# Optimization experiments

Measured on AMD Instinct MI355X. Metric: run time of the kernel, lower is better.

The kernel has to match this reference:

```python
import jax, jax.numpy as jnp
import numpy as np

NODE_SIZE = 128
EDGE_SIZE = 20
CUTOFF = 5.0
N_NODES = 20000
N_EDGES = 600000


def silu(x):
    return x * jax.nn.sigmoid(x)


def setup_inputs() -> dict:
    key = jax.random.key(0)
    ks = jax.random.split(key, 20)
    d = NODE_SIZE
    inp = {
        "node_states_scalar": jax.random.normal(ks[0], (N_NODES, d), jnp.float32),
        "node_states_vector": jax.random.normal(ks[1], (N_NODES, 3, d), jnp.float32),
        "edge_states": jax.random.normal(ks[2], (N_EDGES, EDGE_SIZE), jnp.float32),
        "edge_vectors": jax.random.normal(ks[3], (N_EDGES, 3), jnp.float32),
        "edge_norms": jax.random.uniform(ks[4], (N_EDGES, 1), jnp.float32),
        "edge_index": jax.random.randint(ks[5], (N_EDGES, 2), 0, N_NODES, jnp.int64 if jax.config.jax_enable_x64 else jnp.int32),
        # parameters, stored as [in, out] so y = x @ W + b
        "Wf": jax.random.normal(ks[6], (EDGE_SIZE, 3 * d), jnp.float32) * 0.05,
        "bf": jnp.zeros((3 * d,), jnp.float32),
        "Wm1": jax.random.normal(ks[7], (d, d), jnp.float32) * 0.05,
        "bm1": jnp.zeros((d,), jnp.float32),
        "Wm2": jax.random.normal(ks[8], (d, 3 * d), jnp.float32) * 0.05,
        "bm2": jnp.zeros((3 * d,), jnp.float32),
        "WU": jax.random.normal(ks[9], (d, d), jnp.float32) * 0.05,
        "WV": jax.random.normal(ks[10], (d, d), jnp.float32) * 0.05,
        "Wa1": jax.random.normal(ks[11], (2 * d, d), jnp.float32) * 0.05,
        "ba1": jnp.zeros((d,), jnp.float32),
        "Wa2": jax.random.normal(ks[12], (d, 3 * d), jnp.float32) * 0.05,
        "ba2": jnp.zeros((3 * d,), jnp.float32),
    }
    return inp


def reference(node_states_scalar, node_states_vector, edge_states, edge_vectors,
              edge_norms, edge_index, Wf, bf, Wm1, bm1, Wm2, bm2, WU, WV,
              Wa1, ba1, Wa2, ba2):
    d = NODE_SIZE
    n = node_states_scalar.shape[0]

    # --- message function ---
    # cosine cutoff: 0.5*(cos(pi*r/cutoff)+1) for r < cutoff, else 0
    fc = 0.5 * (jnp.cos(jnp.pi * edge_norms / CUTOFF) + 1.0)
    fc = jnp.where(edge_norms < CUTOFF, fc, 0.0)                      # [E,1]
    filter_weight = (edge_states @ Wf + bf) * fc                      # [E,3d]
    scalar_output = silu(node_states_scalar @ Wm1 + bm1) @ Wm2 + bm2  # [N,3d]

    src = edge_index[:, 0]
    dst = edge_index[:, 1]
    filter_output = filter_weight * scalar_output[src]                # [E,3d]
    gate_nodes = filter_output[:, :d]
    gate_edges = filter_output[:, d:2 * d]
    messages_scalar = filter_output[:, 2 * d:]

    gated_node_vec = node_states_vector[src] * gate_nodes[:, None, :]     # [E,3,d]
    gated_edge_vec = gate_edges[:, None, :] * edge_vectors[:, :, None]    # [E,3,d]
    messages_vector = gated_node_vec + gated_edge_vec

    ds_m = jax.ops.segment_sum(messages_scalar, dst, num_segments=n)  # [N,d]
    dv_m = jax.ops.segment_sum(messages_vector, dst, num_segments=n)  # [N,3,d]

    s = node_states_scalar + ds_m
    v = node_states_vector + dv_m

    # --- node state update ---
    Uv = jnp.einsum('nvd,de->nve', v, WU)
    Vv = jnp.einsum('nvd,de->nve', v, WV)
    Vv_sq = jnp.sum(Vv ** 2, axis=1)                                  # [N,d]
    a = silu(jnp.concatenate([s, Vv_sq], axis=1) @ Wa1 + ba1) @ Wa2 + ba2
    a_ss, a_sv, a_vv = a[:, :d], a[:, d:2 * d], a[:, 2 * d:]
    ip = jnp.sum(Uv * Vv, axis=1)                                     # [N,d]

    s = s + a_ss + a_sv * ip
    v = v + a_vv[:, None, :] * Uv
    return (s, v)
```

## Files before the change

kernel.cpp:

```cpp
#include <hip/hip_runtime.h>

#define ND 128
#define ESZ 20
#define NN 20000
#define NE 600000
#define PI_F 3.14159265358979323846f
#define CUT 5.0f

using short8 = __attribute__((ext_vector_type(8))) short;
using f32x4  = __attribute__((ext_vector_type(4))) float;
using hh2    = __attribute__((ext_vector_type(2))) _Float16;

__device__ __forceinline__ float silu_f(float x) { return x / (1.0f + __expf(-x)); }

__device__ __forceinline__ unsigned short f2bf(float x) {
    unsigned u = __float_as_uint(x);
    unsigned r = (u + 0x7FFFu + ((u >> 16) & 1u)) >> 16;
    return (unsigned short)r;
}
__device__ __forceinline__ float bf2f(unsigned short h) {
    return __uint_as_float(((unsigned)h) << 16);
}
__device__ __forceinline__ unsigned pack2bf(float x, float y) {
    return (unsigned)f2bf(x) | ((unsigned)f2bf(y) << 16);
}
__device__ __forceinline__ unsigned pack2h(float x, float y) {
    _Float16 a = (_Float16)x, b = (_Float16)y;
    unsigned short ua = __builtin_bit_cast(unsigned short, a);
    unsigned short ub = __builtin_bit_cast(unsigned short, b);
    return (unsigned)ua | ((unsigned)ub << 16);
}
__device__ __forceinline__ float dot2u(unsigned a, hh2 b, float acc) {
    return __builtin_amdgcn_fdot2(__builtin_bit_cast(hh2, a), b, acc, false);
}

__device__ __forceinline__ void pack_w(const float* __restrict__ W,
                                       unsigned short* __restrict__ P,
                                       int s, int K, int N) {
    int k = s / N, n = s - k * N;
    int dst = ((((n >> 4) * (K >> 5) + (k >> 5)) * 64) +
               (((k >> 3) & 3) << 4) + (n & 15)) * 8 + (k & 7);
    P[dst] = f2bf(W[s]);
}

#define R0 1920000L
#define R1 (R0 + 180224L)
#define R2 (R1 + 4224L)
#define R3 (R2 + 600000L)

__global__ __launch_bounds__(256) void k_front(
    const float4* __restrict__ ns4, const float4* __restrict__ nsv4,
    const int* __restrict__ eidx,
    const float* __restrict__ Wf, const float* __restrict__ bfb,
    const float* __restrict__ Wm1, const float* __restrict__ Wm2,
    const float* __restrict__ WU, const float* __restrict__ WV,
    const float* __restrict__ Wa1, const float* __restrict__ Wa2,
    float4* __restrict__ outs4, float4* __restrict__ outv4,
    ushort4* __restrict__ nsb4, unsigned* __restrict__ gnh,
    unsigned short* __restrict__ p1, unsigned short* __restrict__ p2,
    unsigned short* __restrict__ pU, unsigned short* __restrict__ pV,
    unsigned short* __restrict__ pa1, unsigned short* __restrict__ pa2,
    unsigned* __restrict__ wfh, int* __restrict__ counts) {
    long gid = (long)blockIdx.x * 256 + threadIdx.x;
    if (gid < R0) {
        long i = gid;
        const long S4 = (long)NN * ND / 4;
        if (i < S4) {
            float4 v = ns4[i];
            outs4[i] = v;
            ushort4 h; h.x = f2bf(v.x); h.y = f2bf(v.y); h.z = f2bf(v.z); h.w = f2bf(v.w);
            nsb4[i] = h;
        }
        float4 w = nsv4[i];
        outv4[i] = w;
        unsigned short* gs = (unsigned short*)gnh;
        long b = i * 4;
        gs[(b + 0) * 2 + 1] = f2bf(w.x);
        gs[(b + 1) * 2 + 1] = f2bf(w.y);
        gs[(b + 2) * 2 + 1] = f2bf(w.z);
        gs[(b + 3) * 2 + 1] = f2bf(w.w);
    } else if (gid < R1) {
        int i = (int)(gid - R0);
        if      (i <  16384) pack_w(Wm1, p1, i,          128, 128);
        else if (i <  65536) pack_w(Wm2, p2, i - 16384,  128, 384);
        else if (i <  81920) pack_w(WU,  pU, i - 65536,  128, 128);
        else if (i <  98304) pack_w(WV,  pV, i - 81920,  128, 128);
        else if (i < 131072) pack_w(Wa1, pa1, i - 98304, 256, 128);
        else                 pack_w(Wa2, pa2, i - 131072,128, 384);
    } else if (gid < R2) {
        int j = (int)(gid - R1);
        int p = j / 384, cc = j - p * 384;
        float a = 0.f, b = 0.f;
        if (p < 10) { a = Wf[(2 * p) * 384 + cc]; b = Wf[(2 * p + 1) * 384 + cc]; }
        else if (p == 10) { a = bfb[cc]; }
        wfh[p * 384 + cc] = pack2h(a, b);
    } else if (gid < R3) {
        int e = (int)(gid - R2);
        atomicAdd(&counts[eidx[2 * e + 1]], 1);
    }
}

#define SCAN_T 1024
__global__ __launch_bounds__(SCAN_T) void k_scan(const int* __restrict__ counts,
                                                 int* __restrict__ offsets,
                                                 int* __restrict__ cursor) {
    __shared__ int part[SCAN_T];
    const int t = threadIdx.x;
    const int CPT = (NN + SCAN_T - 1) / SCAN_T;
    const int base = t * CPT;
    int sum = 0;
    for (int i = 0; i < CPT; ++i) {
        int idx = base + i;
        if (idx < NN) sum += counts[idx];
    }
    part[t] = sum;
    __syncthreads();
    for (int off = 1; off < SCAN_T; off <<= 1) {
        int v = (t >= off) ? part[t - off] : 0;
        __syncthreads();
        part[t] += v;
        __syncthreads();
    }
    int run = (t == 0) ? 0 : part[t - 1];
    for (int i = 0; i < CPT; ++i) {
        int idx = base + i;
        if (idx < NN) {
            offsets[idx] = run;
            cursor[idx] = run;
            run += counts[idx];
        }
    }
    if (t == SCAN_T - 1) offsets[NN] = run;
}

#define SCAT_B 2344
__global__ __launch_bounds__(256) void k_sm(
    const int* __restrict__ eidx, int* __restrict__ cursor,
    const float* __restrict__ es, const float* __restrict__ enorm,
    const float* __restrict__ evec, unsigned* __restrict__ rec,
    const unsigned short* __restrict__ nsb,
    const unsigned short* __restrict__ Wm1p, const float* __restrict__ bm1,
    const unsigned short* __restrict__ Wm2p, const float* __restrict__ bm2,
    unsigned* __restrict__ gnh) {
    __shared__ unsigned short lsh[4][16][136];
    if (blockIdx.x < SCAT_B) {
        int e = blockIdx.x * 256 + threadIdx.x;
        if (e < NE) {
            int s  = eidx[2 * e];
            int dd = eidx[2 * e + 1];
            float nrm = enorm[e];
            float fc = (nrm < CUT) ? 0.5f * (__cosf(PI_F * nrm * (1.0f / CUT)) + 1.0f) : 0.0f;
            const float* er = es + (long)e * ESZ;
            unsigned qv[11];
#pragma unroll
            for (int p = 0; p < 10; ++p)
                qv[p] = pack2h(er[2 * p] * fc, er[2 * p + 1] * fc);
            qv[10] = pack2h(fc, 0.f);
            float e0 = evec[3 * e + 0], e1 = evec[3 * e + 1], e2 = evec[3 * e + 2];
            int pos = atomicAdd(&cursor[dd], 1);
            uint4* rp = (uint4*)rec + (long)pos * 4;
            rp[0] = make_uint4((unsigned)s, (unsigned)dd,
                               __float_as_uint(e0), __float_as_uint(e1));
            rp[1] = make_uint4(__float_as_uint(e2), qv[0], qv[1], qv[2]);
            rp[2] = make_uint4(qv[3], qv[4], qv[5], qv[6]);
            rp[3] = make_uint4(qv[7], qv[8], qv[9], qv[10]);
        }
        return;
    }
    const int lane = threadIdx.x & 63;
    const int wv = threadIdx.x >> 6;
    const int wid = (blockIdx.x - SCAT_B) * 4 + wv;
    const int m0 = wid * 16;
    if (m0 >= NN) return;
    const int ml = lane & 15, q = lane >> 4;

    short8 a1[4];
#pragma unroll
    for (int kb = 0; kb < 4; ++kb)
        a1[kb] = *(const short8*)(nsb + (long)(m0 + ml) * ND + kb * 32 + q * 8);

#pragma unroll
    for (int nt = 0; nt < 8; ++nt) {
        float b = bm1[nt * 16 + ml];
        f32x4 acc = {b, b, b, b};
#pragma unroll
        for (int kb = 0; kb < 4; ++kb) {
            short8 bf = *(const short8*)(Wm1p + ((nt * 4 + kb) * 64 + lane) * 8);
            acc = __builtin_amdgcn_mfma_f32_16x16x32_bf16(a1[kb], bf, acc, 0, 0, 0);
        }
#pragma unroll
        for (int r = 0; r < 4; ++r)
            lsh[wv][q * 4 + r][nt * 16 + ml] = f2bf(silu_f(acc[r]));
    }
    __syncthreads();

    short8 a2[4];
#pragma unroll
    for (int kb = 0; kb < 4; ++kb)
        a2[kb] = *(const short8*)(&lsh[wv][ml][kb * 32 + q * 8]);

    unsigned short* gs = (unsigned short*)gnh;
#pragma unroll
    for (int nt = 0; nt < 24; ++nt) {
        float b = bm2[nt * 16 + ml];
        f32x4 acc = {b, b, b, b};
#pragma unroll
        for (int kb = 0; kb < 4; ++kb) {
            short8 bf = *(const short8*)(Wm2p + ((nt * 4 + kb) * 64 + lane) * 8);
            acc = __builtin_amdgcn_mfma_f32_16x16x32_bf16(a2[kb], bf, acc, 0, 0, 0);
        }
#pragma unroll
        for (int r = 0; r < 4; ++r) {
            long idx = (long)(m0 + q * 4 + r) * 384 + nt * 16 + ml;
            gs[idx * 2] = f2bf(acc[r]);
        }
    }
}

#define NGRP 7500
#define RUN 80
#define SLOTS 8

#define STEP(k, dk, gsrc) {                                                   \
    if ((dk) != cur_dst) {                                                    \
        PUSH();                                                               \
        cur_dst = (dk);                                                       \
        as = 0.f; av0 = 0.f; av1 = 0.f; av2 = 0.f;                            \
    }                                                                         \
    const uint4 M0_ = pp[(k) & 1][0], M1_ = pp[(k) & 1][1],                   \
                M2_ = pp[(k) & 1][2], M3_ = pp[(k) & 1][3];                   \
    const unsigned XA_ = xr[(k) & 7][0], XB_ = xr[(k) & 7][1],                \
                   XC_ = xr[(k) & 7][2];                                      \
                                            \
    { const unsigned* pb_ = (((k) + 2 < 16) ? bc : bn) + ((((k) + 2) & 15) << 4); \
      pp[(k) & 1][0] = *(const uint4*)(pb_);                                  \
      pp[(k) & 1][1] = *(const uint4*)(pb_ + 4);                              \
      pp[(k) & 1][2] = *(const uint4*)(pb_ + 8);                              \
      pp[(k) & 1][3] = *(const uint4*)(pb_ + 12); }                           \
                                                         \
    { const unsigned* gp_ = gnh + (long)(gsrc) * 384;                         \
      xr[(k) & 7][0] = gp_[t];                                                \
      xr[(k) & 7][1] = gp_[128 + t];                                          \
      xr[(k) & 7][2] = gp_[256 + t]; }                                        \
    unsigned ea_[11] = {M1_.y, M1_.z, M1_.w, M2_.x, M2_.y, M2_.z, M2_.w,      \
                        M3_.x, M3_.y, M3_.z, M3_.w};                          \
    float f0 = 0.f, f1 = 0.f, f2 = 0.f;                                       \
    _Pragma("unroll")                                                         \
    for (int p = 0; p < 11; ++p) {                                            \
        f0 = dot2u(ea_[p], wf[p][0], f0);                                     \
        f1 = dot2u(ea_[p], wf[p][1], f1);                                     \
        f2 = dot2u(ea_[p], wf[p][2], f2);                                     \
    }                                                                         \
    f0 *= __uint_as_float(XA_ << 16);                                         \
    f1 *= __uint_as_float(XB_ << 16);                                         \
    f2 *= __uint_as_float(XC_ << 16);                                         \
    as  += f2;                                                                \
    av0 += __uint_as_float(XA_ & 0xffff0000u) * f0 + f1 * __uint_as_float(M0_.z); \
    av1 += __uint_as_float(XB_ & 0xffff0000u) * f0 + f1 * __uint_as_float(M0_.w); \
    av2 += __uint_as_float(XC_ & 0xffff0000u) * f0 + f1 * __uint_as_float(M1_.x); \
}

#define RL(v, j) __builtin_amdgcn_readlane((int)(v), (j))

__global__ __launch_bounds__(256, 3) void k_edge8(
    const unsigned* __restrict__ rec, const unsigned* __restrict__ wfh,
    const unsigned* __restrict__ gnh,
    float* __restrict__ out_s, float* __restrict__ out_v) {
    __shared__ __align__(16) unsigned eb[4][2][256];
    __shared__ float fsl[4][SLOTS][4][64];
    __shared__ int dsl[4][SLOTS];
    const int wv = threadIdx.x >> 6;
    const int lane = threadIdx.x & 63;
    const int grp = blockIdx.x * 2 + (wv >> 1);
    const int t = ((wv & 1) << 6) | lane;
    const long beg = (long)grp * RUN;

    hh2 wf[11][3];
#pragma unroll
    for (int p = 0; p < 11; ++p)
#pragma unroll
        for (int c = 0; c < 3; ++c)
            wf[p][c] = __builtin_bit_cast(hh2, wfh[p * 384 + c * 128 + t]);

    unsigned* const b0 = &eb[wv][0][0];
    unsigned* const b1 = &eb[wv][1][0];

    uint4 sA = *(const uint4*)(rec + (beg + 0)  * 16 + lane * 4);
    uint4 sB = *(const uint4*)(rec + (beg + 16) * 16 + lane * 4);
    uint4 st = *(const uint4*)(rec + (beg + 32) * 16 + lane * 4);
    *(uint4*)&b0[lane * 4] = sA;
    *(uint4*)&b1[lane * 4] = sB;
    uint2 sdC = *(const uint2*)&b0[(lane & 15) << 4];
    uint2 sdN = *(const uint2*)&b1[(lane & 15) << 4];

    uint4 pp[2][4];
    pp[0][0] = *(const uint4*)(b0 + 0);  pp[0][1] = *(const uint4*)(b0 + 4);
    pp[0][2] = *(const uint4*)(b0 + 8);  pp[0][3] = *(const uint4*)(b0 + 12);
    pp[1][0] = *(const uint4*)(b0 + 16); pp[1][1] = *(const uint4*)(b0 + 20);
    pp[1][2] = *(const uint4*)(b0 + 24); pp[1][3] = *(const uint4*)(b0 + 28);

    unsigned xr[8][3];
#define IG(j) { int s_ = RL(sdC.x, j);                                        \
                const unsigned* gp_ = gnh + (long)s_ * 384;                   \
                xr[j][0] = gp_[t]; xr[j][1] = gp_[128 + t];                   \
                xr[j][2] = gp_[256 + t]; }
    IG(0) IG(1) IG(2) IG(3) IG(4) IG(5) IG(6) IG(7)
#undef IG

    int cur_dst = -1;
    int nseg = 0;
    float as = 0.f, av0 = 0.f, av1 = 0.f, av2 = 0.f;

    auto DRAIN = [&]() {
        for (int i = 0; i < nseg; ++i) {
            int d = dsl[wv][i];
            atomicAdd(&out_s[(long)d * ND + t],            fsl[wv][i][0][lane]);
            atomicAdd(&out_v[(long)d * 384 + 0 * ND + t],  fsl[wv][i][1][lane]);
            atomicAdd(&out_v[(long)d * 384 + 1 * ND + t],  fsl[wv][i][2][lane]);
            atomicAdd(&out_v[(long)d * 384 + 2 * ND + t],  fsl[wv][i][3][lane]);
        }
        nseg = 0;
    };
    auto PUSH = [&]() {
        if (cur_dst >= 0) {
            fsl[wv][nseg][0][lane] = as;
            fsl[wv][nseg][1][lane] = av0;
            fsl[wv][nseg][2][lane] = av1;
            fsl[wv][nseg][3][lane] = av2;
            if (lane == 0) dsl[wv][nseg] = cur_dst;
            ++nseg;
            if (nseg == SLOTS) DRAIN();
        }
    };

    for (int c = 0; c < 5; ++c) {
        unsigned* const bc = &eb[wv][c & 1][0];
        unsigned* const bn = &eb[wv][(c + 1) & 1][0];
        const int d0  = RL(sdC.y, 0),  d1  = RL(sdC.y, 1);
        const int d2  = RL(sdC.y, 2),  d3  = RL(sdC.y, 3);
        const int d4  = RL(sdC.y, 4),  d5  = RL(sdC.y, 5);
        const int d6  = RL(sdC.y, 6),  d7  = RL(sdC.y, 7);
        const int d8  = RL(sdC.y, 8),  d9  = RL(sdC.y, 9);
        const int d10 = RL(sdC.y, 10), d11 = RL(sdC.y, 11);
        const int d12 = RL(sdC.y, 12), d13 = RL(sdC.y, 13);
        const int d14 = RL(sdC.y, 14), d15 = RL(sdC.y, 15);
        const int s8  = RL(sdC.x, 8),  s9  = RL(sdC.x, 9);
        const int s10 = RL(sdC.x, 10), s11 = RL(sdC.x, 11);
        const int s12 = RL(sdC.x, 12), s13 = RL(sdC.x, 13);
        const int s14 = RL(sdC.x, 14), s15 = RL(sdC.x, 15);

        STEP(0, d0, s8)   STEP(1, d1, s9)   STEP(2, d2, s10)  STEP(3, d3, s11)
        STEP(4, d4, s12)  STEP(5, d5, s13)  STEP(6, d6, s14)  STEP(7, d7, s15)

        const int gm = (c < 4) ? -1 : 0;
        const int n0 = RL(sdN.x, 0) & gm, n1 = RL(sdN.x, 1) & gm;
        const int n2 = RL(sdN.x, 2) & gm, n3 = RL(sdN.x, 3) & gm;
        const int n4 = RL(sdN.x, 4) & gm, n5 = RL(sdN.x, 5) & gm;
        const int n6 = RL(sdN.x, 6) & gm, n7 = RL(sdN.x, 7) & gm;

        STEP(8,  d8,  n0)  STEP(9,  d9,  n1)  STEP(10, d10, n2) STEP(11, d11, n3)
        STEP(12, d12, n4)  STEP(13, d13, n5)  STEP(14, d14, n6) STEP(15, d15, n7)

        if (c < 4) {
            *(uint4*)&bc[lane * 4] = st;
            st = *(const uint4*)(rec + (beg + (long)(c + 3) * 16) * 16 + lane * 4);
            sdC = sdN;
            sdN = *(const uint2*)&bc[(lane & 15) << 4];
        }
    }
    PUSH();
    DRAIN();
}

__global__ __launch_bounds__(256) void k_tail(
    const unsigned short* __restrict__ WUp, const unsigned short* __restrict__ WVp,
    const unsigned short* __restrict__ Wa1p, const float* __restrict__ ba1,
    const unsigned short* __restrict__ Wa2p, const float* __restrict__ ba2,
    float* __restrict__ out_s, float* __restrict__ out_v) {
    const int lane = threadIdx.x & 63;
    const int wv = threadIdx.x >> 6;
    const int wid = blockIdx.x * 4 + wv;
    const int m0 = wid * 16;
    if (m0 >= NN) return;
    const int ml = lane & 15, q = lane >> 4;
    __shared__ unsigned short ct[4][16][264];
    __shared__ unsigned short hl[4][16][136];

#pragma unroll
    for (int j = 0; j < 16; ++j) {
        int idx = j * 64 + lane;
        int n = idx >> 6, c2 = idx & 63;
        float2 sv = *(const float2*)(out_s + (long)(m0 + n) * 128 + c2 * 2);
        *(unsigned*)&ct[wv][n][c2 * 2] = pack2bf(sv.x, sv.y);
    }

    short8 av[3][4];
#pragma unroll
    for (int ax = 0; ax < 3; ++ax)
#pragma unroll
        for (int kb = 0; kb < 4; ++kb) {
            const float* p = out_v + (long)(m0 + ml) * 384 + ax * 128 + kb * 32 + q * 8;
            float4 x = *(const float4*)p;
            float4 y = *(const float4*)(p + 4);
            short8 s;
            s[0] = (short)f2bf(x.x); s[1] = (short)f2bf(x.y);
            s[2] = (short)f2bf(x.z); s[3] = (short)f2bf(x.w);
            s[4] = (short)f2bf(y.x); s[5] = (short)f2bf(y.y);
            s[6] = (short)f2bf(y.z); s[7] = (short)f2bf(y.w);
            av[ax][kb] = s;
        }

    f32x4 ipr[8];
    unsigned upk[8][3][2];
#pragma unroll
    for (int nt = 0; nt < 8; ++nt) {
        f32x4 u0 = {0.f,0.f,0.f,0.f}, u1 = u0, u2 = u0;
        f32x4 v0 = u0, v1 = u0, v2 = u0;
#pragma unroll
        for (int kb = 0; kb < 4; ++kb) {
            short8 bu = *(const short8*)(WUp + ((nt * 4 + kb) * 64 + lane) * 8);
            short8 bv = *(const short8*)(WVp + ((nt * 4 + kb) * 64 + lane) * 8);
            u0 = __builtin_amdgcn_mfma_f32_16x16x32_bf16(av[0][kb], bu, u0, 0, 0, 0);
            u1 = __builtin_amdgcn_mfma_f32_16x16x32_bf16(av[1][kb], bu, u1, 0, 0, 0);
            u2 = __builtin_amdgcn_mfma_f32_16x16x32_bf16(av[2][kb], bu, u2, 0, 0, 0);
            v0 = __builtin_amdgcn_mfma_f32_16x16x32_bf16(av[0][kb], bv, v0, 0, 0, 0);
            v1 = __builtin_amdgcn_mfma_f32_16x16x32_bf16(av[1][kb], bv, v1, 0, 0, 0);
            v2 = __builtin_amdgcn_mfma_f32_16x16x32_bf16(av[2][kb], bv, v2, 0, 0, 0);
        }
        const int c = nt * 16 + ml;
#pragma unroll
        for (int r = 0; r < 4; ++r) {
            float vs  = v0[r] * v0[r] + v1[r] * v1[r] + v2[r] * v2[r];
            ct[wv][q * 4 + r][128 + c] = f2bf(vs);
            ipr[nt][r] = u0[r] * v0[r] + u1[r] * v1[r] + u2[r] * v2[r];
        }
        upk[nt][0][0] = pack2bf(u0[0], u0[1]); upk[nt][0][1] = pack2bf(u0[2], u0[3]);
        upk[nt][1][0] = pack2bf(u1[0], u1[1]); upk[nt][1][1] = pack2bf(u1[2], u1[3]);
        upk[nt][2][0] = pack2bf(u2[0], u2[1]); upk[nt][2][1] = pack2bf(u2[2], u2[3]);
    }

    short8 a1[8];
#pragma unroll
    for (int kb = 0; kb < 8; ++kb)
        a1[kb] = *(const short8*)(&ct[wv][ml][kb * 32 + q * 8]);

#pragma unroll
    for (int nt = 0; nt < 8; ++nt) {
        float b = ba1[nt * 16 + ml];
        f32x4 acc = {b, b, b, b};
#pragma unroll
        for (int kb = 0; kb < 8; ++kb) {
            short8 bf = *(const short8*)(Wa1p + ((nt * 8 + kb) * 64 + lane) * 8);
            acc = __builtin_amdgcn_mfma_f32_16x16x32_bf16(a1[kb], bf, acc, 0, 0, 0);
        }
#pragma unroll
        for (int r = 0; r < 4; ++r)
            hl[wv][q * 4 + r][nt * 16 + ml] = f2bf(silu_f(acc[r]));
    }

    short8 h[4];
#pragma unroll
    for (int kb = 0; kb < 4; ++kb)
        h[kb] = *(const short8*)(&hl[wv][ml][kb * 32 + q * 8]);

#pragma unroll
    for (int nt = 0; nt < 8; ++nt) {
        float b0 = ba2[nt * 16 + ml];
        float b1 = ba2[128 + nt * 16 + ml];
        f32x4 aS = {b0, b0, b0, b0};
        f32x4 aG = {b1, b1, b1, b1};
#pragma unroll
        for (int kb = 0; kb < 4; ++kb) {
            short8 bS = *(const short8*)(Wa2p + (((nt) * 4 + kb) * 64 + lane) * 8);
            short8 bG = *(const short8*)(Wa2p + (((nt + 8) * 4 + kb) * 64 + lane) * 8);
            aS = __builtin_amdgcn_mfma_f32_16x16x32_bf16(h[kb], bS, aS, 0, 0, 0);
            aG = __builtin_amdgcn_mfma_f32_16x16x32_bf16(h[kb], bG, aG, 0, 0, 0);
        }
#pragma unroll
        for (int r = 0; r < 4; ++r) {
            long grow = m0 + q * 4 + r;
            long o = grow * 128 + nt * 16 + ml;
            out_s[o] = out_s[o] + aS[r] + aG[r] * ipr[nt][r];
        }
    }

#pragma unroll
    for (int nt = 0; nt < 8; ++nt) {
        float b2 = ba2[256 + nt * 16 + ml];
        f32x4 aV = {b2, b2, b2, b2};
#pragma unroll
        for (int kb = 0; kb < 4; ++kb) {
            short8 bV = *(const short8*)(Wa2p + (((nt + 16) * 4 + kb) * 64 + lane) * 8);
            aV = __builtin_amdgcn_mfma_f32_16x16x32_bf16(h[kb], bV, aV, 0, 0, 0);
        }
#pragma unroll
        for (int r = 0; r < 4; ++r) {
            long grow = m0 + q * 4 + r;
            int c = nt * 16 + ml;
#pragma unroll
            for (int ax = 0; ax < 3; ++ax) {
                unsigned pk = upk[nt][ax][r >> 1];
                unsigned short uh = (r & 1) ? (unsigned short)(pk >> 16)
                                            : (unsigned short)(pk & 0xffffu);
                long o = grow * 384 + ax * 128 + c;
                out_v[o] = out_v[o] + aV[r] * bf2f(uh);
            }
        }
    }
}

extern "C" void kernel_launch(void* const* d_in, const int* in_sizes, int n_in,
                              void* d_out, int out_size, void* d_ws, size_t ws_size,
                              hipStream_t stream) {
    const float* ns    = (const float*)d_in[0];
    const float* nsv   = (const float*)d_in[1];
    const float* es    = (const float*)d_in[2];
    const float* evec  = (const float*)d_in[3];
    const float* enorm = (const float*)d_in[4];
    const int*   eidx  = (const int*)d_in[5];
    const float* Wf    = (const float*)d_in[6];
    const float* bfb   = (const float*)d_in[7];
    const float* Wm1   = (const float*)d_in[8];
    const float* bm1   = (const float*)d_in[9];
    const float* Wm2   = (const float*)d_in[10];
    const float* bm2   = (const float*)d_in[11];
    const float* WU    = (const float*)d_in[12];
    const float* WV    = (const float*)d_in[13];
    const float* Wa1   = (const float*)d_in[14];
    const float* ba1   = (const float*)d_in[15];
    const float* Wa2   = (const float*)d_in[16];
    const float* ba2   = (const float*)d_in[17];

    float* out_s = (float*)d_out;
    float* out_v = out_s + (size_t)NN * ND;

    char* w = (char*)d_ws;
    unsigned short* p1  = (unsigned short*)(w + 0);
    unsigned short* p2  = (unsigned short*)(w + 32768);
    unsigned short* pU  = (unsigned short*)(w + 131072);
    unsigned short* pV  = (unsigned short*)(w + 163840);
    unsigned short* pa1 = (unsigned short*)(w + 196608);
    unsigned short* pa2 = (unsigned short*)(w + 262144);
    unsigned* wfh = (unsigned*)(w + 360448);
    int* counts = (int*)(w + 377344);
    int* offs   = (int*)(w + 457344);
    int* cursor = (int*)(w + 537408);
    unsigned* rec = (unsigned*)(w + 617408);
    char* u0 = w + 39024576;
    unsigned* gnh       = (unsigned*)(u0);
    unsigned short* nsb = (unsigned short*)(u0 + 30720000);

    hipMemsetAsync(counts, 0, (size_t)NN * sizeof(int), stream);
    hipMemsetAsync(rec + (size_t)NE * 16, 0, 112 * 64, stream);
    k_front<<<(int)((R3 + 255) / 256), 256, 0, stream>>>(
        (const float4*)ns, (const float4*)nsv, eidx, Wf, bfb,
        Wm1, Wm2, WU, WV, Wa1, Wa2,
        (float4*)out_s, (float4*)out_v, (ushort4*)nsb, gnh,
        p1, p2, pU, pV, pa1, pa2, wfh, counts);
    k_scan<<<1, SCAN_T, 0, stream>>>(counts, offs, cursor);
    k_sm<<<SCAT_B + 313, 256, 0, stream>>>(eidx, cursor, es, enorm, evec, rec,
                                           nsb, p1, bm1, p2, bm2, gnh);
    k_edge8<<<NGRP / 2, 256, 0, stream>>>(rec, wfh, gnh, out_s, out_v);
    k_tail<<<313, 256, 0, stream>>>(pU, pV, pa1, ba1, pa2, ba2, out_s, out_v);
}
```

Baseline: 482.2 us.

## Partition edge kernel by destination nodes to replace atomics with direct writes

Result: slower. 527.5 us (+9.4%).

```diff
diff --git a/kernel.cpp b/kernel.cpp
--- a/kernel.cpp
+++ b/kernel.cpp
@@ -55,7 +55,6 @@
     const float* __restrict__ Wm1, const float* __restrict__ Wm2,
     const float* __restrict__ WU, const float* __restrict__ WV,
     const float* __restrict__ Wa1, const float* __restrict__ Wa2,
-    float4* __restrict__ outs4, float4* __restrict__ outv4,
     ushort4* __restrict__ nsb4, unsigned* __restrict__ gnh,
     unsigned short* __restrict__ p1, unsigned short* __restrict__ p2,
     unsigned short* __restrict__ pU, unsigned short* __restrict__ pV,
@@ -67,12 +66,10 @@
         const long S4 = (long)NN * ND / 4;
         if (i < S4) {
             float4 v = ns4[i];
-            outs4[i] = v;
             ushort4 h; h.x = f2bf(v.x); h.y = f2bf(v.y); h.z = f2bf(v.z); h.w = f2bf(v.w);
             nsb4[i] = h;
         }
         float4 w = nsv4[i];
-        outv4[i] = w;
         unsigned short* gs = (unsigned short*)gnh;
         long b = i * 4;
         gs[(b + 0) * 2 + 1] = f2bf(w.x);
@@ -217,31 +214,29 @@
     }
 }
 
-#define NGRP 7500
-#define RUN 80
-#define SLOTS 8
-
-#define STEP(k, dk, gsrc) {                                                   \
-    if ((dk) != cur_dst) {                                                    \
-        PUSH();                                                               \
-        cur_dst = (dk);                                                       \
+#define NDST 4
+#define EMAX 192
+#define NGRP9 (NN / NDST)
+
+#define RL(v, j) __builtin_amdgcn_readlane((int)(v), (j))
+
+#define FLS(sg) {                                                             \
+    fsl[gl][sg][0][t] = as;                                                   \
+    fsl[gl][sg][1][t] = av0;                                                  \
+    fsl[gl][sg][2][t] = av1;                                                  \
+    fsl[gl][sg][3][t] = av2;                                                  \
+}
+
+#define BCHK(k) {                                                             \
+    while ((k) == b_next) {                                                   \
+        FLS(seg);                                                             \
         as = 0.f; av0 = 0.f; av1 = 0.f; av2 = 0.f;                            \
+        ++seg;                                                                \
+        b_next = (seg == 1) ? B2 : (seg == 2) ? B3 : 0x7fffffff;              \
     }                                                                         \
-    const uint4 M0_ = pp[(k) & 1][0], M1_ = pp[(k) & 1][1],                   \
-                M2_ = pp[(k) & 1][2], M3_ = pp[(k) & 1][3];                   \
-    const unsigned XA_ = xr[(k) & 7][0], XB_ = xr[(k) & 7][1],                \
-                   XC_ = xr[(k) & 7][2];                                      \
-                                            \
-    { const unsigned* pb_ = (((k) + 2 < 16) ? bc : bn) + ((((k) + 2) & 15) << 4); \
-      pp[(k) & 1][0] = *(const uint4*)(pb_);                                  \
-      pp[(k) & 1][1] = *(const uint4*)(pb_ + 4);                              \
-      pp[(k) & 1][2] = *(const uint4*)(pb_ + 8);                              \
-      pp[(k) & 1][3] = *(const uint4*)(pb_ + 12); }                           \
-                                                         \
-    { const unsigned* gp_ = gnh + (long)(gsrc) * 384;                         \
-      xr[(k) & 7][0] = gp_[t];                                                \
-      xr[(k) & 7][1] = gp_[128 + t];                                          \
-      xr[(k) & 7][2] = gp_[256 + t]; }                                        \
+}
+
+#define ECOMP(M0_, M1_, M2_, M3_, XA_, XB_, XC_) {                            \
     unsigned ea_[11] = {M1_.y, M1_.z, M1_.w, M2_.x, M2_.y, M2_.z, M2_.w,      \
                         M3_.x, M3_.y, M3_.z, M3_.w};                          \
     float f0 = 0.f, f1 = 0.f, f2 = 0.f;                                       \
@@ -260,20 +255,39 @@
     av2 += __uint_as_float(XC_ & 0xffff0000u) * f0 + f1 * __uint_as_float(M1_.x); \
 }
 
-#define RL(v, j) __builtin_amdgcn_readlane((int)(v), (j))
-
-__global__ __launch_bounds__(256, 3) void k_edge8(
+#define ESTEP(k, s) {                                                         \
+    BCHK(k)                                                                   \
+    const uint4 M0_ = pq[(s) & 1][0], M1_ = pq[(s) & 1][1],                   \
+                M2_ = pq[(s) & 1][2], M3_ = pq[(s) & 1][3];                   \
+    const unsigned XA_ = xr[s][0], XB_ = xr[s][1], XC_ = xr[s][2];            \
+    { const int kp_ = (k) + 2;                                                \
+      const unsigned* pa_ = (kp_ < fl) ? rb + (long)kp_ * 16 : zrec;          \
+      pq[(s) & 1][0] = *(const uint4*)(pa_);                                  \
+      pq[(s) & 1][1] = *(const uint4*)(pa_ + 4);                              \
+      pq[(s) & 1][2] = *(const uint4*)(pa_ + 8);                              \
+      pq[(s) & 1][3] = *(const uint4*)(pa_ + 12); }                           \
+    { int kg_ = (k) + 4; if (kg_ > EMAX - 1) kg_ = EMAX - 1;                  \
+      const int ln_ = kg_ & 63;                                               \
+      int sg_ = RL(srcA, ln_);                                                \
+      sg_ = (kg_ >= 64)  ? RL(srcB, ln_) : sg_;                               \
+      sg_ = (kg_ >= 128) ? RL(srcC, ln_) : sg_;                               \
+      const unsigned* gp_ = gnh + (long)sg_ * 384;                            \
+      xr[s][0] = gp_[t]; xr[s][1] = gp_[128 + t]; xr[s][2] = gp_[256 + t]; }  \
+    ECOMP(M0_, M1_, M2_, M3_, XA_, XB_, XC_)                                  \
+}
+
+__global__ __launch_bounds__(256, 4) void k_edge9(
     const unsigned* __restrict__ rec, const unsigned* __restrict__ wfh,
-    const unsigned* __restrict__ gnh,
+    const unsigned* __restrict__ gnh, const int* __restrict__ offs,
+    const float* __restrict__ ns, const float* __restrict__ nsv,
     float* __restrict__ out_s, float* __restrict__ out_v) {
-    __shared__ __align__(16) unsigned eb[4][2][256];
-    __shared__ float fsl[4][SLOTS][4][64];
-    __shared__ int dsl[4][SLOTS];
+    __shared__ float fsl[2][NDST][4][128];
     const int wv = threadIdx.x >> 6;
     const int lane = threadIdx.x & 63;
-    const int grp = blockIdx.x * 2 + (wv >> 1);
+    const int gl = wv >> 1;
+    const int grp = blockIdx.x * 2 + gl;
     const int t = ((wv & 1) << 6) | lane;
-    const long beg = (long)grp * RUN;
+    const int d0n = grp * NDST;
 
     hh2 wf[11][3];
 #pragma unroll
@@ -282,94 +296,79 @@
         for (int c = 0; c < 3; ++c)
             wf[p][c] = __builtin_bit_cast(hh2, wfh[p * 384 + c * 128 + t]);
 
-    unsigned* const b0 = &eb[wv][0][0];
-    unsigned* const b1 = &eb[wv][1][0];
-
-    uint4 sA = *(const uint4*)(rec + (beg + 0)  * 16 + lane * 4);
-    uint4 sB = *(const uint4*)(rec + (beg + 16) * 16 + lane * 4);
-    uint4 st = *(const uint4*)(rec + (beg + 32) * 16 + lane * 4);
-    *(uint4*)&b0[lane * 4] = sA;
-    *(uint4*)&b1[lane * 4] = sB;
-    uint2 sdC = *(const uint2*)&b0[(lane & 15) << 4];
-    uint2 sdN = *(const uint2*)&b1[(lane & 15) << 4];
-
-    uint4 pp[2][4];
-    pp[0][0] = *(const uint4*)(b0 + 0);  pp[0][1] = *(const uint4*)(b0 + 4);
-    pp[0][2] = *(const uint4*)(b0 + 8);  pp[0][3] = *(const uint4*)(b0 + 12);
-    pp[1][0] = *(const uint4*)(b0 + 16); pp[1][1] = *(const uint4*)(b0 + 20);
-    pp[1][2] = *(const uint4*)(b0 + 24); pp[1][3] = *(const uint4*)(b0 + 28);
-
-    unsigned xr[8][3];
-#define IG(j) { int s_ = RL(sdC.x, j);                                        \
-                const unsigned* gp_ = gnh + (long)s_ * 384;                   \
-                xr[j][0] = gp_[t]; xr[j][1] = gp_[128 + t];                   \
-                xr[j][2] = gp_[256 + t]; }
-    IG(0) IG(1) IG(2) IG(3) IG(4) IG(5) IG(6) IG(7)
-#undef IG
-
-    int cur_dst = -1;
-    int nseg = 0;
+    const int boff = offs[d0n];
+    const int B1 = offs[d0n + 1] - boff;
+    const int B2 = offs[d0n + 2] - boff;
+    const int B3 = offs[d0n + 3] - boff;
+    const int len = offs[d0n + 4] - boff;
+    const unsigned* rb = rec + (long)boff * 16;
+    const unsigned* zrec = rec + (long)NE * 16;
+
+    unsigned srcA = rb[lane * 16];
+    unsigned srcB = rb[(lane + 64) * 16];
+    unsigned srcC = rb[(lane + 128) * 16];
+
+    const int fl = (len < EMAX) ? len : EMAX;
+
+    uint4 pq[2][4];
+    {
+        const unsigned* pa0 = (0 < fl) ? rb : zrec;
+        const unsigned* pa1 = (1 < fl) ? rb + 16 : zrec;
+        pq[0][0] = *(const uint4*)(pa0);      pq[0][1] = *(const uint4*)(pa0 + 4);
+        pq[0][2] = *(const uint4*)(pa0 + 8);  pq[0][3] = *(const uint4*)(pa0 + 12);
+        pq[1][0] = *(const uint4*)(pa1);      pq[1][1] = *(const uint4*)(pa1 + 4);
+        pq[1][2] = *(const uint4*)(pa1 + 8);  pq[1][3] = *(const uint4*)(pa1 + 12);
+    }
+    unsigned xr[4][3];
+#pragma unroll
+    for (int k = 0; k < 4; ++k) {
+        int sgp = RL(srcA, k);
+        const unsigned* gp = gnh + (long)sgp * 384;
+        xr[k][0] = gp[t]; xr[k][1] = gp[128 + t]; xr[k][2] = gp[256 + t];
+    }
+
+    int seg = 0;
+    int b_next = B1;
     float as = 0.f, av0 = 0.f, av1 = 0.f, av2 = 0.f;
 
-    auto DRAIN = [&]() {
-        for (int i = 0; i < nseg; ++i) {
-            int d = dsl[wv][i];
-            atomicAdd(&out_s[(long)d * ND + t],            fsl[wv][i][0][lane]);
-            atomicAdd(&out_v[(long)d * 384 + 0 * ND + t],  fsl[wv][i][1][lane]);
-            atomicAdd(&out_v[(long)d * 384 + 1 * ND + t],  fsl[wv][i][2][lane]);
-            atomicAdd(&out_v[(long)d * 384 + 2 * ND + t],  fsl[wv][i][3][lane]);
-        }
-        nseg = 0;
-    };
-    auto PUSH = [&]() {
-        if (cur_dst >= 0) {
-            fsl[wv][nseg][0][lane] = as;
-            fsl[wv][nseg][1][lane] = av0;
-            fsl[wv][nseg][2][lane] = av1;
-            fsl[wv][nseg][3][lane] = av2;
-            if (lane == 0) dsl[wv][nseg] = cur_dst;
-            ++nseg;
-            if (nseg == SLOTS) DRAIN();
-        }
-    };
-
-    for (int c = 0; c < 5; ++c) {
-        unsigned* const bc = &eb[wv][c & 1][0];
-        unsigned* const bn = &eb[wv][(c + 1) & 1][0];
-        const int d0  = RL(sdC.y, 0),  d1  = RL(sdC.y, 1);
-        const int d2  = RL(sdC.y, 2),  d3  = RL(sdC.y, 3);
-        const int d4  = RL(sdC.y, 4),  d5  = RL(sdC.y, 5);
-        const int d6  = RL(sdC.y, 6),  d7  = RL(sdC.y, 7);
-        const int d8  = RL(sdC.y, 8),  d9  = RL(sdC.y, 9);
-        const int d10 = RL(sdC.y, 10), d11 = RL(sdC.y, 11);
-        const int d12 = RL(sdC.y, 12), d13 = RL(sdC.y, 13);
-        const int d14 = RL(sdC.y, 14), d15 = RL(sdC.y, 15);
-        const int s8  = RL(sdC.x, 8),  s9  = RL(sdC.x, 9);
-        const int s10 = RL(sdC.x, 10), s11 = RL(sdC.x, 11);
-        const int s12 = RL(sdC.x, 12), s13 = RL(sdC.x, 13);
-        const int s14 = RL(sdC.x, 14), s15 = RL(sdC.x, 15);
-
-        STEP(0, d0, s8)   STEP(1, d1, s9)   STEP(2, d2, s10)  STEP(3, d3, s11)
-        STEP(4, d4, s12)  STEP(5, d5, s13)  STEP(6, d6, s14)  STEP(7, d7, s15)
-
-        const int gm = (c < 4) ? -1 : 0;
-        const int n0 = RL(sdN.x, 0) & gm, n1 = RL(sdN.x, 1) & gm;
-        const int n2 = RL(sdN.x, 2) & gm, n3 = RL(sdN.x, 3) & gm;
-        const int n4 = RL(sdN.x, 4) & gm, n5 = RL(sdN.x, 5) & gm;
-        const int n6 = RL(sdN.x, 6) & gm, n7 = RL(sdN.x, 7) & gm;
-
-        STEP(8,  d8,  n0)  STEP(9,  d9,  n1)  STEP(10, d10, n2) STEP(11, d11, n3)
-        STEP(12, d12, n4)  STEP(13, d13, n5)  STEP(14, d14, n6) STEP(15, d15, n7)
-
-        if (c < 4) {
-            *(uint4*)&bc[lane * 4] = st;
-            st = *(const uint4*)(rec + (beg + (long)(c + 3) * 16) * 16 + lane * 4);
-            sdC = sdN;
-            sdN = *(const uint2*)&bc[(lane & 15) << 4];
-        }
-    }
-    PUSH();
-    DRAIN();
+    const int nit = (fl + 3) >> 2;
+#pragma clang loop unroll(disable)
+    for (int it = 0; it < nit; ++it) {
+        const int k0 = it * 4;
+        ESTEP(k0 + 0, 0)
+        ESTEP(k0 + 1, 1)
+        ESTEP(k0 + 2, 2)
+        ESTEP(k0 + 3, 3)
+    }
+
+    if (len > EMAX) {
+        for (int k = EMAX; k < len; ++k) {
+            BCHK(k)
+            const unsigned* pa = rb + (long)k * 16;
+            uint4 m0 = *(const uint4*)(pa),     m1 = *(const uint4*)(pa + 4);
+            uint4 m2 = *(const uint4*)(pa + 8), m3 = *(const uint4*)(pa + 12);
+            const unsigned* gp = gnh + (long)m0.x * 384;
+            unsigned xa = gp[t], xb = gp[128 + t], xc = gp[256 + t];
+            ECOMP(m0, m1, m2, m3, xa, xb, xc)
+        }
+    }
+
+    FLS(seg);
+    as = 0.f; av0 = 0.f; av1 = 0.f; av2 = 0.f;
+    for (int i = seg + 1; i < NDST; ++i) FLS(i);
+
+#pragma unroll
+    for (int d = 0; d < NDST; ++d) {
+        const long node = d0n + d;
+        float s0 = fsl[gl][d][0][t];
+        float v0 = fsl[gl][d][1][t];
+        float v1 = fsl[gl][d][2][t];
+        float v2 = fsl[gl][d][3][t];
+        out_s[node * ND + t]            = ns[node * ND + t] + s0;
+        out_v[node * 384 + 0 * ND + t]  = nsv[node * 384 + 0 * ND + t] + v0;
+        out_v[node * 384 + 1 * ND + t]  = nsv[node * 384 + 1 * ND + t] + v1;
+        out_v[node * 384 + 2 * ND + t]  = nsv[node * 384 + 2 * ND + t] + v2;
+    }
 }
 
 __global__ __launch_bounds__(256) void k_tail(
@@ -546,20 +545,21 @@
     int* offs   = (int*)(w + 457344);
     int* cursor = (int*)(w + 537408);
     unsigned* rec = (unsigned*)(w + 617408);
-    char* u0 = w + 39024576;
+    char* u0 = w + 39029696;
     unsigned* gnh       = (unsigned*)(u0);
     unsigned short* nsb = (unsigned short*)(u0 + 30720000);
 
     hipMemsetAsync(counts, 0, (size_t)NN * sizeof(int), stream);
-    hipMemsetAsync(rec + (size_t)NE * 16, 0, 112 * 64, stream);
+    hipMemsetAsync(rec + (size_t)NE * 16, 0, 192 * 64, stream);
     k_front<<<(int)((R3 + 255) / 256), 256, 0, stream>>>(
         (const float4*)ns, (const float4*)nsv, eidx, Wf, bfb,
         Wm1, Wm2, WU, WV, Wa1, Wa2,
-        (float4*)out_s, (float4*)out_v, (ushort4*)nsb, gnh,
+        (ushort4*)nsb, gnh,
         p1, p2, pU, pV, pa1, pa2, wfh, counts);
     k_scan<<<1, SCAN_T, 0, stream>>>(counts, offs, cursor);
     k_sm<<<SCAT_B + 313, 256, 0, stream>>>(eidx, cursor, es, enorm, evec, rec,
                                            nsb, p1, bm1, p2, bm2, gnh);
-    k_edge8<<<NGRP / 2, 256, 0, stream>>>(rec, wfh, gnh, out_s, out_v);
+    k_edge9<<<NGRP9 / 2, 256, 0, stream>>>(rec, wfh, gnh, offs, ns, nsv,
+                                           out_s, out_v);
     k_tail<<<313, 256, 0, stream>>>(pU, pV, pa1, ba1, pa2, ba2, out_s, out_v);
 }
```

## Pack node-vector bf16 into gnh in k_sm and flush edge segments directly

Applied to the files above, without the earlier changes.

After: 468.0 us. 2.9% less time.

```diff
diff --git a/kernel.cpp b/kernel.cpp
--- a/kernel.cpp
+++ b/kernel.cpp
@@ -56,7 +56,7 @@
     const float* __restrict__ WU, const float* __restrict__ WV,
     const float* __restrict__ Wa1, const float* __restrict__ Wa2,
     float4* __restrict__ outs4, float4* __restrict__ outv4,
-    ushort4* __restrict__ nsb4, unsigned* __restrict__ gnh,
+    ushort4* __restrict__ nsb4,
     unsigned short* __restrict__ p1, unsigned short* __restrict__ p2,
     unsigned short* __restrict__ pU, unsigned short* __restrict__ pV,
     unsigned short* __restrict__ pa1, unsigned short* __restrict__ pa2,
@@ -71,14 +71,7 @@
             ushort4 h; h.x = f2bf(v.x); h.y = f2bf(v.y); h.z = f2bf(v.z); h.w = f2bf(v.w);
             nsb4[i] = h;
         }
-        float4 w = nsv4[i];
-        outv4[i] = w;
-        unsigned short* gs = (unsigned short*)gnh;
-        long b = i * 4;
-        gs[(b + 0) * 2 + 1] = f2bf(w.x);
-        gs[(b + 1) * 2 + 1] = f2bf(w.y);
-        gs[(b + 2) * 2 + 1] = f2bf(w.z);
-        gs[(b + 3) * 2 + 1] = f2bf(w.w);
+        outv4[i] = nsv4[i];
     } else if (gid < R1) {
         int i = (int)(gid - R0);
         if      (i <  16384) pack_w(Wm1, p1, i,          128, 128);
@@ -138,7 +131,7 @@
     const int* __restrict__ eidx, int* __restrict__ cursor,
     const float* __restrict__ es, const float* __restrict__ enorm,
     const float* __restrict__ evec, unsigned* __restrict__ rec,
-    const unsigned short* __restrict__ nsb,
+    const unsigned short* __restrict__ nsb, const float* __restrict__ nsv,
     const unsigned short* __restrict__ Wm1p, const float* __restrict__ bm1,
     const unsigned short* __restrict__ Wm2p, const float* __restrict__ bm2,
     unsigned* __restrict__ gnh) {
@@ -199,7 +192,6 @@
     for (int kb = 0; kb < 4; ++kb)
         a2[kb] = *(const short8*)(&lsh[wv][ml][kb * 32 + q * 8]);
 
-    unsigned short* gs = (unsigned short*)gnh;
 #pragma unroll
     for (int nt = 0; nt < 24; ++nt) {
         float b = bm2[nt * 16 + ml];
@@ -212,19 +204,25 @@
 #pragma unroll
         for (int r = 0; r < 4; ++r) {
             long idx = (long)(m0 + q * 4 + r) * 384 + nt * 16 + ml;
-            gs[idx * 2] = f2bf(acc[r]);
+            gnh[idx] = (unsigned)f2bf(acc[r]) | ((unsigned)f2bf(nsv[idx]) << 16);
         }
     }
 }
 
 #define NGRP 7500
 #define RUN 80
-#define SLOTS 8
+
+#define FLUSH() {                                                             \
+    atomicAdd(&out_s[(long)cur_dst * ND + t], as);                            \
+    atomicAdd(&out_v[(long)cur_dst * 384 + 0 * ND + t], av0);                 \
+    atomicAdd(&out_v[(long)cur_dst * 384 + 1 * ND + t], av1);                 \
+    atomicAdd(&out_v[(long)cur_dst * 384 + 2 * ND + t], av2);                 \
+}
 
 #define STEP(k, dk, gsrc) {                                                   \
-    if ((dk) != cur_dst) {                                                    \
-        PUSH();                                                               \
-        cur_dst = (dk);                                                       \
+    if (dk != cur_dst) {                                                      \
+        if (cur_dst >= 0) FLUSH();                                            \
+        cur_dst = dk;                                                         \
         as = 0.f; av0 = 0.f; av1 = 0.f; av2 = 0.f;                            \
     }                                                                         \
     const uint4 M0_ = pp[(k) & 1][0], M1_ = pp[(k) & 1][1],                   \
@@ -262,13 +260,11 @@
 
 #define RL(v, j) __builtin_amdgcn_readlane((int)(v), (j))
 
-__global__ __launch_bounds__(256, 3) void k_edge8(
+__global__ __launch_bounds__(256, 3) void k_edge7(
     const unsigned* __restrict__ rec, const unsigned* __restrict__ wfh,
     const unsigned* __restrict__ gnh,
     float* __restrict__ out_s, float* __restrict__ out_v) {
     __shared__ __align__(16) unsigned eb[4][2][256];
-    __shared__ float fsl[4][SLOTS][4][64];
-    __shared__ int dsl[4][SLOTS];
     const int wv = threadIdx.x >> 6;
     const int lane = threadIdx.x & 63;
     const int grp = blockIdx.x * 2 + (wv >> 1);
@@ -308,30 +304,7 @@
 #undef IG
 
     int cur_dst = -1;
-    int nseg = 0;
     float as = 0.f, av0 = 0.f, av1 = 0.f, av2 = 0.f;
-
-    auto DRAIN = [&]() {
-        for (int i = 0; i < nseg; ++i) {
-            int d = dsl[wv][i];
-            atomicAdd(&out_s[(long)d * ND + t],            fsl[wv][i][0][lane]);
-            atomicAdd(&out_v[(long)d * 384 + 0 * ND + t],  fsl[wv][i][1][lane]);
-            atomicAdd(&out_v[(long)d * 384 + 1 * ND + t],  fsl[wv][i][2][lane]);
-            atomicAdd(&out_v[(long)d * 384 + 2 * ND + t],  fsl[wv][i][3][lane]);
-        }
-        nseg = 0;
-    };
-    auto PUSH = [&]() {
-        if (cur_dst >= 0) {
-            fsl[wv][nseg][0][lane] = as;
-            fsl[wv][nseg][1][lane] = av0;
-            fsl[wv][nseg][2][lane] = av1;
-            fsl[wv][nseg][3][lane] = av2;
-            if (lane == 0) dsl[wv][nseg] = cur_dst;
-            ++nseg;
-            if (nseg == SLOTS) DRAIN();
-        }
-    };
 
     for (int c = 0; c < 5; ++c) {
         unsigned* const bc = &eb[wv][c & 1][0];
@@ -368,8 +341,7 @@
             sdN = *(const uint2*)&bc[(lane & 15) << 4];
         }
     }
-    PUSH();
-    DRAIN();
+    FLUSH();
 }
 
 __global__ __launch_bounds__(256) void k_tail(
@@ -555,11 +527,11 @@
     k_front<<<(int)((R3 + 255) / 256), 256, 0, stream>>>(
         (const float4*)ns, (const float4*)nsv, eidx, Wf, bfb,
         Wm1, Wm2, WU, WV, Wa1, Wa2,
-        (float4*)out_s, (float4*)out_v, (ushort4*)nsb, gnh,
+        (float4*)out_s, (float4*)out_v, (ushort4*)nsb,
         p1, p2, pU, pV, pa1, pa2, wfh, counts);
     k_scan<<<1, SCAN_T, 0, stream>>>(counts, offs, cursor);
     k_sm<<<SCAT_B + 313, 256, 0, stream>>>(eidx, cursor, es, enorm, evec, rec,
-                                           nsb, p1, bm1, p2, bm2, gnh);
-    k_edge8<<<NGRP / 2, 256, 0, stream>>>(rec, wfh, gnh, out_s, out_v);
+                                           nsb, nsv, p1, bm1, p2, bm2, gnh);
+    k_edge7<<<NGRP / 2, 256, 0, stream>>>(rec, wfh, gnh, out_s, out_v);
     k_tail<<<313, 256, 0, stream>>>(pU, pV, pa1, ba1, pa2, ba2, out_s, out_v);
 }
```
